# Optimization experiments

Measured on AMD Instinct MI355X. Metric: run time of the kernel, lower is better.

Reference implementation:

```python
import jax, jax.numpy as jnp
import numpy as np

B = 64; PAST = 128; FUTURE = 64; HID = 64; HEADS = 4
F = 16 + 8 + 24 + 3  # out_preprocess = 51


def _pre(cat, num, emb0, emb1, emb2):
    # pre_processing: embedding lookups per categorical column + last 3 float cols
    return jnp.concatenate([emb0[cat[:, 0]], emb1[cat[:, 1]], emb2[cat[:, 2]], num], axis=-1)


def _gat_conv(x, edge_index, lin_w, att_src, att_dst, bias, heads, out_ch):
    # PyG GATConv: concat=False (head mean), add_self_loops=True, leaky_relu slope 0.2
    N = x.shape[0]
    loops = jnp.arange(N, dtype=edge_index.dtype)
    src = jnp.concatenate([edge_index[0], loops])
    dst = jnp.concatenate([edge_index[1], loops])
    h = (x @ lin_w).reshape(N, heads, out_ch)          # [N, H, C]
    a_src = (h * att_src).sum(-1)                      # [N, H]
    a_dst = (h * att_dst).sum(-1)
    e = jax.nn.leaky_relu(a_src[src] + a_dst[dst], 0.2)  # [E, H]
    m = jax.lax.stop_gradient(jax.ops.segment_max(e, dst, num_segments=N))
    ex = jnp.exp(e - m[dst])
    s = jax.ops.segment_sum(ex, dst, num_segments=N)
    alpha = ex / (s[dst] + 1e-16)                      # softmax over in-edges per node
    out = jax.ops.segment_sum(alpha[:, :, None] * h[src], dst, num_segments=N)
    return out.mean(1) + bias                          # concat=False -> mean over heads


def setup_inputs() -> dict:
    ks = jax.random.split(jax.random.key(0), 17)
    N1, N2 = B * PAST, B * FUTURE
    E1, E2 = N1 * 16, N2 * 16
    return dict(
        cat1=jax.random.randint(ks[0], (N1, 3), 0, 7),
        num1=jax.random.normal(ks[1], (N1, 3), dtype=jnp.float32),
        cat2=jax.random.randint(ks[2], (N2, 3), 0, 7),
        num2=jax.random.normal(ks[3], (N2, 3), dtype=jnp.float32),
        e1=jax.random.randint(ks[4], (2, E1), 0, N1),
        e2=jax.random.randint(ks[5], (2, E2), 0, N2),
        A=jax.random.randint(ks[6], (PAST + FUTURE, PAST + FUTURE), 0, 2),
        emb0=0.1 * jax.random.normal(ks[7], (24, 16), dtype=jnp.float32),
        emb1=0.1 * jax.random.normal(ks[8], (7, 8), dtype=jnp.float32),
        emb2=0.1 * jax.random.normal(ks[9], (500, 24), dtype=jnp.float32),
        g1_lin=0.1 * jax.random.normal(ks[10], (F, HEADS * (F - 1)), dtype=jnp.float32),
        g1_asrc=0.1 * jax.random.normal(ks[11], (HEADS, F - 1), dtype=jnp.float32),
        g1_adst=0.1 * jax.random.normal(ks[12], (HEADS, F - 1), dtype=jnp.float32),
        g1_b=jnp.zeros((F - 1,), dtype=jnp.float32),
        g2_lin=0.1 * jax.random.normal(ks[13], (F, HEADS), dtype=jnp.float32),
        g2_asrc=0.1 * jax.random.normal(ks[14], (HEADS, 1), dtype=jnp.float32),
        g2_adst=0.1 * jax.random.normal(ks[15], (HEADS, 1), dtype=jnp.float32),
        g2_b=jnp.zeros((1,), dtype=jnp.float32),
        W=0.1 * jax.random.normal(ks[16], (F - 1, HID), dtype=jnp.float32),
    )


def reference(cat1, num1, cat2, num2, e1, e2, A, emb0, emb1, emb2,
              g1_lin, g1_asrc, g1_adst, g1_b, g2_lin, g2_asrc, g2_adst, g2_b, W):
    x = _pre(cat1, num1, emb0, emb1, emb2)                       # [B*PAST, F]
    x2 = _pre(cat2, num2, emb0, emb1, emb2).reshape(B, FUTURE, F)
    x1 = _gat_conv(x, e1, g1_lin, g1_asrc, g1_adst, g1_b, HEADS, F - 1).reshape(B, PAST, F - 1)
    # pairwise diff between every (future, past) node pair within a graph
    diff = x1[:, None, :, :] - x2[:, :, None, :F - 1]            # [B, FUTURE, PAST, F-1]
    M = W @ W.T
    M = M + M.T                                                  # WW^T + (WW^T)^T
    # original builds full [PAST, PAST] quadratic form and extracts diagonal;
    # compute only the diagonal: -0.5 * diff_i M diff_i
    alpha = -0.5 * jnp.einsum('bfpd,de,bfpe->bfp', diff, M, diff)
    mask = A[:PAST, PAST:].T                                     # [FUTURE, PAST]
    alpha = jnp.where(mask == 0, -jnp.inf, alpha)
    alpha = jax.nn.softmax(alpha, axis=-1)
    y_past = x.reshape(B, PAST, F)[:, :, -1:]                    # [B, PAST, 1]
    tmp = alpha @ y_past                                         # [B, FUTURE, 1]
    x2b = jnp.concatenate([x2[:, :, :F - 1], tmp], axis=-1)
    out = _gat_conv(x2b.reshape(-1, F), e2, g2_lin, g2_asrc, g2_adst, g2_b, HEADS, 1)
    return out.reshape(B, FUTURE)
```

## Files before the change

### kernel.cpp

```cpp
#include <hip/hip_runtime.h>

static constexpr int B_ = 64, PAST = 128, FUTURE = 64, F_ = 51;
static constexpr int N1 = B_ * PAST;
static constexpr int N2 = B_ * FUTURE;
static constexpr int E1 = N1 * 16;
static constexpr int E2 = N2 * 16;
static constexpr int MAXDEG = 64;
static constexpr int CSR_TOT = E1 + N1 + E2 + N2 + FUTURE * PAST;
static constexpr int NB_CSR = CSR_TOT / 256;

__device__ __forceinline__
float node_feat(const int* cat, const float* num, const float* e0, const float* e1,
                const float* e2, int n, int t) {
    if (t < 16) return e0[cat[n * 3 + 0] * 16 + t];
    if (t < 24) return e1[cat[n * 3 + 1] * 8 + (t - 16)];
    if (t < 48) return e2[cat[n * 3 + 2] * 24 + (t - 24)];
    return num[n * 3 + (t - 48)];
}

__global__ __launch_bounds__(256) void k_prep(
        const int* __restrict__ cat1, const float* __restrict__ num1,
        const int* __restrict__ cat2, const float* __restrict__ num2,
        const float* __restrict__ emb0, const float* __restrict__ emb1,
        const float* __restrict__ emb2,
        const float* __restrict__ g1_lin, const float* __restrict__ g1_asrc,
        const float* __restrict__ g1_adst, const float* __restrict__ W,
        const float* __restrict__ g2_lin,
        const int* __restrict__ e1, const int* __restrict__ e2,
        const int* __restrict__ A,
        float* __restrict__ h1, float* __restrict__ asrc1, float* __restrict__ adst1,
        float* __restrict__ y1, float* __restrict__ x2g, float* __restrict__ P2,
        float* __restrict__ h2b,
        int* __restrict__ count1, int* __restrict__ slot1,
        int* __restrict__ count2, int* __restrict__ slot2, int* __restrict__ maskT) {
    int blk = blockIdx.x, t = threadIdx.x;
    if (blk < NB_CSR) {
        int i = blk * 256 + t;
        if (i < E1) {
            int src = e1[i], dst = e1[E1 + i];
            int pos = atomicAdd(&count1[dst], 1);
            if (pos < MAXDEG) slot1[dst * MAXDEG + pos] = src;
        } else if (i < E1 + N1) {
            int n = i - E1;
            int pos = atomicAdd(&count1[n], 1);
            if (pos < MAXDEG) slot1[n * MAXDEG + pos] = n;
        } else if (i < E1 + N1 + E2) {
            int k = i - E1 - N1;
            int src = e2[k], dst = e2[E2 + k];
            int pos = atomicAdd(&count2[dst], 1);
            if (pos < MAXDEG) slot2[dst * MAXDEG + pos] = src;
        } else if (i < E1 + N1 + E2 + N2) {
            int n = i - E1 - N1 - E2;
            int pos = atomicAdd(&count2[n], 1);
            if (pos < MAXDEG) slot2[n * MAXDEG + pos] = n;
        } else if (i < CSR_TOT) {
            int k = i - (E1 + N1 + E2 + N2);
            int f = k >> 7, pp = k & 127;
            maskT[k] = A[pp * 192 + PAST + f];
        }
        return;
    }
    __shared__ float xrow[F_];
    __shared__ float redS[200];
    __shared__ float redD[200];
    int rb = blk - NB_CSR;
    if (rb >= N1) {
        int n = rb - N1;
        if (t < F_) {
            float xv = node_feat(cat2, num2, emb0, emb1, emb2, n, t);
            xrow[t] = xv;
            x2g[n * F_ + t] = xv;
        }
        __syncthreads();
        if (t < 64) {
            float acc = 0.f;
            for (int j = 0; j < 50; ++j) acc += xrow[j] * W[j * 64 + t];
            P2[n * 64 + t] = acc;
        } else if (t < 68) {
            int h = t - 64;
            float acc = 0.f;
            for (int j = 0; j < 50; ++j) acc += xrow[j] * g2_lin[j * 4 + h];
            h2b[n * 4 + h] = acc;
        }
        return;
    }
    int n = rb;
    if (t < F_) {
        float xv = node_feat(cat1, num1, emb0, emb1, emb2, n, t);
        xrow[t] = xv;
        if (t == 50) y1[n] = xv;
    }
    __syncthreads();
    if (t < 200) {
        float acc = 0.f;
        for (int j = 0; j < F_; ++j) acc += xrow[j] * g1_lin[j * 200 + t];
        h1[n * 200 + t] = acc;
        redS[t] = acc * g1_asrc[t];
        redD[t] = acc * g1_adst[t];
    }
    __syncthreads();
    if (t < 4) {
        float s = 0.f;
        for (int c = 0; c < 50; ++c) s += redS[t * 50 + c];
        asrc1[n * 4 + t] = s;
    } else if (t < 8) {
        int h = t - 4;
        float s = 0.f;
        for (int c = 0; c < 50; ++c) s += redD[h * 50 + c];
        adst1[n * 4 + h] = s;
    }
}

__global__ __launch_bounds__(256) void k_gat1(
        const int* __restrict__ count1, const int* __restrict__ slot1,
        const float* __restrict__ h1, const float* __restrict__ asrc1,
        const float* __restrict__ adst1, const float* __restrict__ g1_b,
        const float* __restrict__ W, float* __restrict__ P1T,
        float* __restrict__ n1w) {
    __shared__ int    Ssrc[4][64];
    __shared__ float4 Sw[4][64];
    __shared__ float  Sx[4][64];
    int t = threadIdx.x, lane = t & 63, wv = t >> 6;
    int n = (blockIdx.x * 256 + t) >> 6;
    int deg = min(count1[n], MAXDEG);
    int my_src = (lane < deg) ? slot1[n * MAXDEG + lane] : 0;
    float ad0 = adst1[n * 4 + 0], ad1 = adst1[n * 4 + 1];
    float ad2 = adst1[n * 4 + 2], ad3 = adst1[n * 4 + 3];
    float ex0 = 0.f, ex1 = 0.f, ex2 = 0.f, ex3 = 0.f;
    if (lane < deg) {
        float e0 = asrc1[my_src * 4 + 0] + ad0;
        float e1 = asrc1[my_src * 4 + 1] + ad1;
        float e2 = asrc1[my_src * 4 + 2] + ad2;
        float e3 = asrc1[my_src * 4 + 3] + ad3;
        e0 = e0 >= 0.f ? e0 : 0.2f * e0;  ex0 = __expf(e0);
        e1 = e1 >= 0.f ? e1 : 0.2f * e1;  ex1 = __expf(e1);
        e2 = e2 >= 0.f ? e2 : 0.2f * e2;  ex2 = __expf(e2);
        e3 = e3 >= 0.f ? e3 : 0.2f * e3;  ex3 = __expf(e3);
    }
    float s0 = ex0, s1 = ex1, s2 = ex2, s3 = ex3;
    #pragma unroll
    for (int m = 32; m >= 1; m >>= 1) {
        s0 += __shfl_xor(s0, m);
        s1 += __shfl_xor(s1, m);
        s2 += __shfl_xor(s2, m);
        s3 += __shfl_xor(s3, m);
    }
    Ssrc[wv][lane] = my_src;
    Sw[wv][lane] = make_float4(ex0 / (s0 + 1e-16f), ex1 / (s1 + 1e-16f),
                               ex2 / (s2 + 1e-16f), ex3 / (s3 + 1e-16f));
    __syncthreads();
    float acc0 = 0.f, acc1 = 0.f, acc2 = 0.f, acc3 = 0.f;
    for (int i = 0; i < deg; ++i) {
        int srci = Ssrc[wv][i];
        float4 w = Sw[wv][i];
        if (lane < 50) {
            const float* hr = &h1[srci * 200];
            acc0 += w.x * hr[lane];
            acc1 += w.y * hr[50 + lane];
            acc2 += w.z * hr[100 + lane];
            acc3 += w.w * hr[150 + lane];
        }
    }
    if (lane < 50)
        Sx[wv][lane] = 0.25f * (acc0 + acc1 + acc2 + acc3) + g1_b[lane];
    __syncthreads();
    float a = 0.f;
    for (int j = 0; j < 50; ++j) a += Sx[wv][j] * W[j * 64 + lane];
    int b = n >> 7, p = n & 127;
    P1T[b * 8192 + lane * 128 + p] = a;
    float sq = a * a;
    #pragma unroll
    for (int m = 32; m >= 1; m >>= 1) sq += __shfl_xor(sq, m);
    if (lane == 0) n1w[n] = sq;
}

__global__ __launch_bounds__(256) void k_attn(
        const float* __restrict__ P1T, const float* __restrict__ P2,
        const int* __restrict__ maskT, const float* __restrict__ y1,
        const float* __restrict__ n1w, const float* __restrict__ h2b,
        const float* __restrict__ g2_lin, float* __restrict__ h2g) {
    __shared__ __align__(16) float P1s[8192];
    __shared__ __align__(16) float ys[128];
    __shared__ __align__(16) float n1s[128];
    int b = blockIdx.x >> 4, fg = blockIdx.x & 15;
    int t = threadIdx.x, lane = t & 63, wv = t >> 6;
    const float4* src4 = (const float4*)(P1T + b * 8192);
    float4* dst4 = (float4*)P1s;
    #pragma unroll
    for (int i = 0; i < 8; ++i) dst4[t + i * 256] = src4[t + i * 256];
    if (t < 128) {
        ys[t]  = y1[b * 128 + t];
        n1s[t] = n1w[b * 128 + t];
    }
    __syncthreads();
    int f = (fg << 2) + wv;
    int q = b * 64 + f;
    float p2k = P2[q * 64 + lane];
    float dota = 0.f, dotb = 0.f;
    const float2* P12 = (const float2*)P1s;
    #pragma unroll
    for (int k = 0; k < 64; ++k) {
        float bk = __shfl(p2k, k);
        float2 v = P12[k * 64 + lane];
        dota += v.x * bk;
        dotb += v.y * bk;
    }
    int2  mm  = ((const int2*)maskT)[f * 64 + lane];
    float2 nv = ((const float2*)n1s)[lane];
    float va = mm.x ? (2.f * dota - nv.x) : -1e30f;
    float vb = mm.y ? (2.f * dotb - nv.y) : -1e30f;
    float mx = fmaxf(va, vb);
    #pragma unroll
    for (int m = 32; m >= 1; m >>= 1) mx = fmaxf(mx, __shfl_xor(mx, m));
    float wa = mm.x ? __expf(va - mx) : 0.f;
    float wb = mm.y ? __expf(vb - mx) : 0.f;
    float2 yv = ((const float2*)ys)[lane];
    float sw = wa + wb;
    float sy = wa * yv.x + wb * yv.y;
    #pragma unroll
    for (int m = 32; m >= 1; m >>= 1) {
        sw += __shfl_xor(sw, m);
        sy += __shfl_xor(sy, m);
    }
    float tsh = sy / sw;
    if (lane < 4)
        h2g[q * 4 + lane] = h2b[q * 4 + lane] + tsh * g2_lin[50 * 4 + lane];
}

__global__ __launch_bounds__(256) void k_gat2(
        const int* __restrict__ count2, const int* __restrict__ slot2,
        const float* __restrict__ h2g, const float* __restrict__ g2_asrc,
        const float* __restrict__ g2_adst, const float* __restrict__ g2_b,
        float* __restrict__ out) {
    int wave = (blockIdx.x * blockDim.x + threadIdx.x) >> 6;
    int lane = threadIdx.x & 63;
    if (wave >= N2) return;
    int n = wave;
    int deg = min(count2[n], MAXDEG);
    int my_src = (lane < deg) ? slot2[n * MAXDEG + lane] : 0;
    float ex[4], nm[4], adterm[4], as[4];
    #pragma unroll
    for (int h = 0; h < 4; ++h) {
        as[h] = g2_asrc[h];
        adterm[h] = h2g[n * 4 + h] * g2_adst[h];
        ex[h] = 0.f; nm[h] = 0.f;
    }
    if (lane < deg) {
        #pragma unroll
        for (int h = 0; h < 4; ++h) {
            float hs = h2g[my_src * 4 + h];
            float e = hs * as[h] + adterm[h];
            e = e >= 0.f ? e : 0.2f * e;
            float xv = __expf(e);
            ex[h] = xv;
            nm[h] = xv * hs;
        }
    }
    #pragma unroll
    for (int m = 32; m >= 1; m >>= 1) {
        #pragma unroll
        for (int h = 0; h < 4; ++h) {
            ex[h] += __shfl_xor(ex[h], m);
            nm[h] += __shfl_xor(nm[h], m);
        }
    }
    if (lane == 0) {
        float o = 0.f;
        #pragma unroll
        for (int h = 0; h < 4; ++h) o += nm[h] / (ex[h] + 1e-16f);
        out[n] = 0.25f * o + g2_b[0];
    }
}

extern "C" void kernel_launch(void* const* d_in, const int* in_sizes, int n_in,
                              void* d_out, int out_size, void* d_ws, size_t ws_size,
                              hipStream_t stream) {
    const int*   cat1    = (const int*)  d_in[0];
    const float* num1    = (const float*)d_in[1];
    const int*   cat2    = (const int*)  d_in[2];
    const float* num2    = (const float*)d_in[3];
    const int*   e1      = (const int*)  d_in[4];
    const int*   e2      = (const int*)  d_in[5];
    const int*   A       = (const int*)  d_in[6];
    const float* emb0    = (const float*)d_in[7];
    const float* emb1    = (const float*)d_in[8];
    const float* emb2    = (const float*)d_in[9];
    const float* g1_lin  = (const float*)d_in[10];
    const float* g1_asrc = (const float*)d_in[11];
    const float* g1_adst = (const float*)d_in[12];
    const float* g1_b    = (const float*)d_in[13];
    const float* g2_lin  = (const float*)d_in[14];
    const float* g2_asrc = (const float*)d_in[15];
    const float* g2_adst = (const float*)d_in[16];
    const float* g2_b    = (const float*)d_in[17];
    const float* W       = (const float*)d_in[18];
    float* out = (float*)d_out;

    int*   count1 = (int*)d_ws;
    int*   count2 = count1 + N1;
    int*   slot1  = count2 + N2;
    int*   slot2  = slot1 + N1 * MAXDEG;
    int*   maskT  = slot2 + N2 * MAXDEG;
    float* h1     = (float*)(maskT + FUTURE * PAST);
    float* asrc1  = h1 + N1 * 200;
    float* adst1  = asrc1 + N1 * 4;
    float* y1     = adst1 + N1 * 4;
    float* x2g    = y1 + N1;
    float* P1T    = x2g + N2 * F_;
    float* P2     = P1T + N1 * 64;
    float* h2g    = P2 + N2 * 64;
    float* n1w    = h2g + N2 * 4;
    float* h2b    = n1w + N1;

    hipMemsetAsync(count1, 0, (N1 + N2) * sizeof(int), stream);
    k_prep<<<NB_CSR + N1 + N2, 256, 0, stream>>>(
        cat1, num1, cat2, num2, emb0, emb1, emb2, g1_lin, g1_asrc, g1_adst, W,
        g2_lin, e1, e2, A, h1, asrc1, adst1, y1, x2g, P2, h2b,
        count1, slot1, count2, slot2, maskT);
    k_gat1<<<N1 / 4, 256, 0, stream>>>(count1, slot1, h1, asrc1, adst1, g1_b, W,
                                       P1T, n1w);
    k_attn<<<B_ * 16, 256, 0, stream>>>(P1T, P2, maskT, y1, n1w, h2b, g2_lin, h2g);
    k_gat2<<<N2 / 4, 256, 0, stream>>>(count2, slot2, h2g, g2_asrc, g2_adst, g2_b, out);
}
```

Baseline: 163.6 us.

## Fuse four kernels into one cooperative persistent kernel with grid syncs

Replaces the four separate launches (prep, gat1, attn, gat2) with a single cooperative persistent kernel that walks each phase with grid-stride loops and separates phases with grid.sync(). The goal is to remove per-launch overhead and the inter-kernel gaps. In exchange the grid is capped at 1024 blocks, so each block loops over many nodes, and grid barriers bring their own cost. The unused x2g buffer write is also dropped. If the cooperative launch fails, the code falls back to four persistent launches.

```diff
diff --git a/kernel.cpp b/kernel.cpp
--- a/kernel.cpp
+++ b/kernel.cpp
@@ -1,4 +1,7 @@
 #include <hip/hip_runtime.h>
+#include <hip/hip_cooperative_groups.h>
+
+namespace cg = cooperative_groups;
 
 static constexpr int B_ = 64, PAST = 128, FUTURE = 64, F_ = 51;
 static constexpr int N1 = B_ * PAST;
@@ -6,8 +9,17 @@
 static constexpr int E1 = N1 * 16;
 static constexpr int E2 = N2 * 16;
 static constexpr int MAXDEG = 64;
-static constexpr int CSR_TOT = E1 + N1 + E2 + N2 + FUTURE * PAST;
-static constexpr int NB_CSR = CSR_TOT / 256;
+static constexpr int CSRW = E1 + N1 + E2 + N2;
+static constexpr int MAXGRID = 1024;
+
+struct GArgs {
+    const int *cat1, *cat2, *e1, *e2, *A;
+    const float *num1, *num2, *emb0, *emb1, *emb2;
+    const float *g1_lin, *g1_asrc, *g1_adst, *g1_b;
+    const float *g2_lin, *g2_asrc, *g2_adst, *g2_b, *W;
+    int *count1, *slot1, *count2, *slot2, *maskT;
+    float *h1, *asrc1, *adst1, *y1, *P2, *h2b, *P1T, *n1w, *h2g, *out;
+};
 
 __device__ __forceinline__
 float node_feat(const int* cat, const float* num, const float* e0, const float* e1,
@@ -18,307 +30,326 @@
     return num[n * 3 + (t - 48)];
 }
 
-__global__ __launch_bounds__(256) void k_prep(
-        const int* __restrict__ cat1, const float* __restrict__ num1,
-        const int* __restrict__ cat2, const float* __restrict__ num2,
-        const float* __restrict__ emb0, const float* __restrict__ emb1,
-        const float* __restrict__ emb2,
-        const float* __restrict__ g1_lin, const float* __restrict__ g1_asrc,
-        const float* __restrict__ g1_adst, const float* __restrict__ W,
-        const float* __restrict__ g2_lin,
-        const int* __restrict__ e1, const int* __restrict__ e2,
-        const int* __restrict__ A,
-        float* __restrict__ h1, float* __restrict__ asrc1, float* __restrict__ adst1,
-        float* __restrict__ y1, float* __restrict__ x2g, float* __restrict__ P2,
-        float* __restrict__ h2b,
-        int* __restrict__ count1, int* __restrict__ slot1,
-        int* __restrict__ count2, int* __restrict__ slot2, int* __restrict__ maskT) {
-    int blk = blockIdx.x, t = threadIdx.x;
-    if (blk < NB_CSR) {
-        int i = blk * 256 + t;
+__device__ void phase_prep(const GArgs& a, float* S) {
+    const int t = threadIdx.x, blk = blockIdx.x;
+    const int nthread = gridDim.x * 256;
+    for (int i = blk * 256 + t; i < CSRW + FUTURE * PAST; i += nthread) {
         if (i < E1) {
-            int src = e1[i], dst = e1[E1 + i];
-            int pos = atomicAdd(&count1[dst], 1);
-            if (pos < MAXDEG) slot1[dst * MAXDEG + pos] = src;
+            int src = a.e1[i], dst = a.e1[E1 + i];
+            int pos = atomicAdd(&a.count1[dst], 1);
+            if (pos < MAXDEG) a.slot1[dst * MAXDEG + pos] = src;
         } else if (i < E1 + N1) {
             int n = i - E1;
-            int pos = atomicAdd(&count1[n], 1);
-            if (pos < MAXDEG) slot1[n * MAXDEG + pos] = n;
+            int pos = atomicAdd(&a.count1[n], 1);
+            if (pos < MAXDEG) a.slot1[n * MAXDEG + pos] = n;
         } else if (i < E1 + N1 + E2) {
             int k = i - E1 - N1;
-            int src = e2[k], dst = e2[E2 + k];
-            int pos = atomicAdd(&count2[dst], 1);
-            if (pos < MAXDEG) slot2[dst * MAXDEG + pos] = src;
-        } else if (i < E1 + N1 + E2 + N2) {
+            int src = a.e2[k], dst = a.e2[E2 + k];
+            int pos = atomicAdd(&a.count2[dst], 1);
+            if (pos < MAXDEG) a.slot2[dst * MAXDEG + pos] = src;
+        } else if (i < CSRW) {
             int n = i - E1 - N1 - E2;
-            int pos = atomicAdd(&count2[n], 1);
-            if (pos < MAXDEG) slot2[n * MAXDEG + pos] = n;
-        } else if (i < CSR_TOT) {
-            int k = i - (E1 + N1 + E2 + N2);
+            int pos = atomicAdd(&a.count2[n], 1);
+            if (pos < MAXDEG) a.slot2[n * MAXDEG + pos] = n;
+        } else {
+            int k = i - CSRW;
             int f = k >> 7, pp = k & 127;
-            maskT[k] = A[pp * 192 + PAST + f];
-        }
-        return;
-    }
-    __shared__ float xrow[F_];
-    __shared__ float redS[200];
-    __shared__ float redD[200];
-    int rb = blk - NB_CSR;
-    if (rb >= N1) {
-        int n = rb - N1;
-        if (t < F_) {
-            float xv = node_feat(cat2, num2, emb0, emb1, emb2, n, t);
-            xrow[t] = xv;
-            x2g[n * F_ + t] = xv;
-        }
+            a.maskT[k] = a.A[pp * 192 + PAST + f];
+        }
+    }
+    float* xrow = S;
+    float* redS = S + 64;
+    float* redD = S + 264;
+    for (int vb = blk; vb < N1 + N2; vb += gridDim.x) {
         __syncthreads();
-        if (t < 64) {
-            float acc = 0.f;
-            for (int j = 0; j < 50; ++j) acc += xrow[j] * W[j * 64 + t];
-            P2[n * 64 + t] = acc;
-        } else if (t < 68) {
-            int h = t - 64;
-            float acc = 0.f;
-            for (int j = 0; j < 50; ++j) acc += xrow[j] * g2_lin[j * 4 + h];
-            h2b[n * 4 + h] = acc;
-        }
-        return;
-    }
-    int n = rb;
-    if (t < F_) {
-        float xv = node_feat(cat1, num1, emb0, emb1, emb2, n, t);
-        xrow[t] = xv;
-        if (t == 50) y1[n] = xv;
-    }
-    __syncthreads();
-    if (t < 200) {
-        float acc = 0.f;
-        for (int j = 0; j < F_; ++j) acc += xrow[j] * g1_lin[j * 200 + t];
-        h1[n * 200 + t] = acc;
-        redS[t] = acc * g1_asrc[t];
-        redD[t] = acc * g1_adst[t];
-    }
-    __syncthreads();
-    if (t < 4) {
-        float s = 0.f;
-        for (int c = 0; c < 50; ++c) s += redS[t * 50 + c];
-        asrc1[n * 4 + t] = s;
-    } else if (t < 8) {
-        int h = t - 4;
-        float s = 0.f;
-        for (int c = 0; c < 50; ++c) s += redD[h * 50 + c];
-        adst1[n * 4 + h] = s;
-    }
-}
-
-__global__ __launch_bounds__(256) void k_gat1(
-        const int* __restrict__ count1, const int* __restrict__ slot1,
-        const float* __restrict__ h1, const float* __restrict__ asrc1,
-        const float* __restrict__ adst1, const float* __restrict__ g1_b,
-        const float* __restrict__ W, float* __restrict__ P1T,
-        float* __restrict__ n1w) {
-    __shared__ int    Ssrc[4][64];
-    __shared__ float4 Sw[4][64];
-    __shared__ float  Sx[4][64];
-    int t = threadIdx.x, lane = t & 63, wv = t >> 6;
-    int n = (blockIdx.x * 256 + t) >> 6;
-    int deg = min(count1[n], MAXDEG);
-    int my_src = (lane < deg) ? slot1[n * MAXDEG + lane] : 0;
-    float ad0 = adst1[n * 4 + 0], ad1 = adst1[n * 4 + 1];
-    float ad2 = adst1[n * 4 + 2], ad3 = adst1[n * 4 + 3];
-    float ex0 = 0.f, ex1 = 0.f, ex2 = 0.f, ex3 = 0.f;
-    if (lane < deg) {
-        float e0 = asrc1[my_src * 4 + 0] + ad0;
-        float e1 = asrc1[my_src * 4 + 1] + ad1;
-        float e2 = asrc1[my_src * 4 + 2] + ad2;
-        float e3 = asrc1[my_src * 4 + 3] + ad3;
-        e0 = e0 >= 0.f ? e0 : 0.2f * e0;  ex0 = __expf(e0);
-        e1 = e1 >= 0.f ? e1 : 0.2f * e1;  ex1 = __expf(e1);
-        e2 = e2 >= 0.f ? e2 : 0.2f * e2;  ex2 = __expf(e2);
-        e3 = e3 >= 0.f ? e3 : 0.2f * e3;  ex3 = __expf(e3);
-    }
-    float s0 = ex0, s1 = ex1, s2 = ex2, s3 = ex3;
-    #pragma unroll
-    for (int m = 32; m >= 1; m >>= 1) {
-        s0 += __shfl_xor(s0, m);
-        s1 += __shfl_xor(s1, m);
-        s2 += __shfl_xor(s2, m);
-        s3 += __shfl_xor(s3, m);
-    }
-    Ssrc[wv][lane] = my_src;
-    Sw[wv][lane] = make_float4(ex0 / (s0 + 1e-16f), ex1 / (s1 + 1e-16f),
+        if (vb < N1) {
+            int n = vb;
+            if (t < F_) {
+                float xv = node_feat(a.cat1, a.num1, a.emb0, a.emb1, a.emb2, n, t);
+                xrow[t] = xv;
+                if (t == 50) a.y1[n] = xv;
+            }
+            __syncthreads();
+            if (t < 200) {
+                float acc = 0.f;
+                for (int j = 0; j < F_; ++j) acc += xrow[j] * a.g1_lin[j * 200 + t];
+                a.h1[n * 200 + t] = acc;
+                redS[t] = acc * a.g1_asrc[t];
+                redD[t] = acc * a.g1_adst[t];
+            }
+            __syncthreads();
+            if (t < 4) {
+                float s = 0.f;
+                for (int c = 0; c < 50; ++c) s += redS[t * 50 + c];
+                a.asrc1[n * 4 + t] = s;
+            } else if (t < 8) {
+                int h = t - 4;
+                float s = 0.f;
+                for (int c = 0; c < 50; ++c) s += redD[h * 50 + c];
+                a.adst1[n * 4 + h] = s;
+            }
+        } else {
+            int n = vb - N1;
+            if (t < F_) {
+                float xv = node_feat(a.cat2, a.num2, a.emb0, a.emb1, a.emb2, n, t);
+                xrow[t] = xv;
+            }
+            __syncthreads();
+            if (t < 64) {
+                float acc = 0.f;
+                for (int j = 0; j < 50; ++j) acc += xrow[j] * a.W[j * 64 + t];
+                a.P2[n * 64 + t] = acc;
+            } else if (t < 68) {
+                int h = t - 64;
+                float acc = 0.f;
+                for (int j = 0; j < 50; ++j) acc += xrow[j] * a.g2_lin[j * 4 + h];
+                a.h2b[n * 4 + h] = acc;
+            }
+        }
+    }
+}
+
+__device__ void phase_gat1(const GArgs& a, float* S) {
+    const int t = threadIdx.x, lane = t & 63, wv = t >> 6;
+    int*    Ssrc = (int*)S + wv * 64;
+    float4* Sw   = (float4*)(S + 256) + wv * 64;
+    float*  Sx   = S + 1280 + wv * 64;
+    const int wstride = gridDim.x * 4;
+    for (int n = blockIdx.x * 4 + wv; n < N1; n += wstride) {
+        int deg = min(a.count1[n], MAXDEG);
+        int my_src = (lane < deg) ? a.slot1[n * MAXDEG + lane] : 0;
+        float ad0 = a.adst1[n * 4 + 0], ad1 = a.adst1[n * 4 + 1];
+        float ad2 = a.adst1[n * 4 + 2], ad3 = a.adst1[n * 4 + 3];
+        float ex0 = 0.f, ex1 = 0.f, ex2 = 0.f, ex3 = 0.f;
+        if (lane < deg) {
+            float e0 = a.asrc1[my_src * 4 + 0] + ad0;
+            float e1 = a.asrc1[my_src * 4 + 1] + ad1;
+            float e2 = a.asrc1[my_src * 4 + 2] + ad2;
+            float e3 = a.asrc1[my_src * 4 + 3] + ad3;
+            e0 = e0 >= 0.f ? e0 : 0.2f * e0;  ex0 = __expf(e0);
+            e1 = e1 >= 0.f ? e1 : 0.2f * e1;  ex1 = __expf(e1);
+            e2 = e2 >= 0.f ? e2 : 0.2f * e2;  ex2 = __expf(e2);
+            e3 = e3 >= 0.f ? e3 : 0.2f * e3;  ex3 = __expf(e3);
+        }
+        float s0 = ex0, s1 = ex1, s2 = ex2, s3 = ex3;
+        #pragma unroll
+        for (int m = 32; m >= 1; m >>= 1) {
+            s0 += __shfl_xor(s0, m);
+            s1 += __shfl_xor(s1, m);
+            s2 += __shfl_xor(s2, m);
+            s3 += __shfl_xor(s3, m);
+        }
+        Ssrc[lane] = my_src;
+        Sw[lane] = make_float4(ex0 / (s0 + 1e-16f), ex1 / (s1 + 1e-16f),
                                ex2 / (s2 + 1e-16f), ex3 / (s3 + 1e-16f));
-    __syncthreads();
-    float acc0 = 0.f, acc1 = 0.f, acc2 = 0.f, acc3 = 0.f;
-    for (int i = 0; i < deg; ++i) {
-        int srci = Ssrc[wv][i];
-        float4 w = Sw[wv][i];
-        if (lane < 50) {
-            const float* hr = &h1[srci * 200];
-            acc0 += w.x * hr[lane];
-            acc1 += w.y * hr[50 + lane];
-            acc2 += w.z * hr[100 + lane];
-            acc3 += w.w * hr[150 + lane];
-        }
-    }
-    if (lane < 50)
-        Sx[wv][lane] = 0.25f * (acc0 + acc1 + acc2 + acc3) + g1_b[lane];
-    __syncthreads();
-    float a = 0.f;
-    for (int j = 0; j < 50; ++j) a += Sx[wv][j] * W[j * 64 + lane];
-    int b = n >> 7, p = n & 127;
-    P1T[b * 8192 + lane * 128 + p] = a;
-    float sq = a * a;
-    #pragma unroll
-    for (int m = 32; m >= 1; m >>= 1) sq += __shfl_xor(sq, m);
-    if (lane == 0) n1w[n] = sq;
-}
-
-__global__ __launch_bounds__(256) void k_attn(
-        const float* __restrict__ P1T, const float* __restrict__ P2,
-        const int* __restrict__ maskT, const float* __restrict__ y1,
-        const float* __restrict__ n1w, const float* __restrict__ h2b,
-        const float* __restrict__ g2_lin, float* __restrict__ h2g) {
-    __shared__ __align__(16) float P1s[8192];
-    __shared__ __align__(16) float ys[128];
-    __shared__ __align__(16) float n1s[128];
-    int b = blockIdx.x >> 4, fg = blockIdx.x & 15;
-    int t = threadIdx.x, lane = t & 63, wv = t >> 6;
-    const float4* src4 = (const float4*)(P1T + b * 8192);
-    float4* dst4 = (float4*)P1s;
-    #pragma unroll
-    for (int i = 0; i < 8; ++i) dst4[t + i * 256] = src4[t + i * 256];
-    if (t < 128) {
-        ys[t]  = y1[b * 128 + t];
-        n1s[t] = n1w[b * 128 + t];
-    }
-    __syncthreads();
-    int f = (fg << 2) + wv;
-    int q = b * 64 + f;
-    float p2k = P2[q * 64 + lane];
-    float dota = 0.f, dotb = 0.f;
-    const float2* P12 = (const float2*)P1s;
-    #pragma unroll
-    for (int k = 0; k < 64; ++k) {
-        float bk = __shfl(p2k, k);
-        float2 v = P12[k * 64 + lane];
-        dota += v.x * bk;
-        dotb += v.y * bk;
-    }
-    int2  mm  = ((const int2*)maskT)[f * 64 + lane];
-    float2 nv = ((const float2*)n1s)[lane];
-    float va = mm.x ? (2.f * dota - nv.x) : -1e30f;
-    float vb = mm.y ? (2.f * dotb - nv.y) : -1e30f;
-    float mx = fmaxf(va, vb);
-    #pragma unroll
-    for (int m = 32; m >= 1; m >>= 1) mx = fmaxf(mx, __shfl_xor(mx, m));
-    float wa = mm.x ? __expf(va - mx) : 0.f;
-    float wb = mm.y ? __expf(vb - mx) : 0.f;
-    float2 yv = ((const float2*)ys)[lane];
-    float sw = wa + wb;
-    float sy = wa * yv.x + wb * yv.y;
-    #pragma unroll
-    for (int m = 32; m >= 1; m >>= 1) {
-        sw += __shfl_xor(sw, m);
-        sy += __shfl_xor(sy, m);
-    }
-    float tsh = sy / sw;
-    if (lane < 4)
-        h2g[q * 4 + lane] = h2b[q * 4 + lane] + tsh * g2_lin[50 * 4 + lane];
-}
-
-__global__ __launch_bounds__(256) void k_gat2(
-        const int* __restrict__ count2, const int* __restrict__ slot2,
-        const float* __restrict__ h2g, const float* __restrict__ g2_asrc,
-        const float* __restrict__ g2_adst, const float* __restrict__ g2_b,
-        float* __restrict__ out) {
-    int wave = (blockIdx.x * blockDim.x + threadIdx.x) >> 6;
-    int lane = threadIdx.x & 63;
-    if (wave >= N2) return;
-    int n = wave;
-    int deg = min(count2[n], MAXDEG);
-    int my_src = (lane < deg) ? slot2[n * MAXDEG + lane] : 0;
-    float ex[4], nm[4], adterm[4], as[4];
-    #pragma unroll
-    for (int h = 0; h < 4; ++h) {
-        as[h] = g2_asrc[h];
-        adterm[h] = h2g[n * 4 + h] * g2_adst[h];
-        ex[h] = 0.f; nm[h] = 0.f;
-    }
-    if (lane < deg) {
+        float acc0 = 0.f, acc1 = 0.f, acc2 = 0.f, acc3 = 0.f;
+        for (int i = 0; i < deg; ++i) {
+            int srci = Ssrc[i];
+            float4 w = Sw[i];
+            if (lane < 50) {
+                const float* hr = &a.h1[srci * 200];
+                acc0 += w.x * hr[lane];
+                acc1 += w.y * hr[50 + lane];
+                acc2 += w.z * hr[100 + lane];
+                acc3 += w.w * hr[150 + lane];
+            }
+        }
+        if (lane < 50)
+            Sx[lane] = 0.25f * (acc0 + acc1 + acc2 + acc3) + a.g1_b[lane];
+        float av = 0.f;
+        for (int j = 0; j < 50; ++j) av += Sx[j] * a.W[j * 64 + lane];
+        int b = n >> 7, p = n & 127;
+        a.P1T[b * 8192 + lane * 128 + p] = av;
+        float sq = av * av;
+        #pragma unroll
+        for (int m = 32; m >= 1; m >>= 1) sq += __shfl_xor(sq, m);
+        if (lane == 0) a.n1w[n] = sq;
+    }
+}
+
+__device__ void phase_attn(const GArgs& a, float* S) {
+    float* P1s = S;
+    float* ys  = S + 8192;
+    float* n1s = S + 8320;
+    const int t = threadIdx.x, lane = t & 63, wv = t >> 6;
+    for (int task = blockIdx.x; task < B_ * 16; task += gridDim.x) {
+        __syncthreads();
+        int b = task >> 4, fg = task & 15;
+        const float4* src4 = (const float4*)(a.P1T + b * 8192);
+        float4* dst4 = (float4*)P1s;
+        #pragma unroll
+        for (int i = 0; i < 8; ++i) dst4[t + i * 256] = src4[t + i * 256];
+        if (t < 128) {
+            ys[t]  = a.y1[b * 128 + t];
+            n1s[t] = a.n1w[b * 128 + t];
+        }
+        __syncthreads();
+        int f = (fg << 2) + wv;
+        int q = b * 64 + f;
+        float p2k = a.P2[q * 64 + lane];
+        float dota = 0.f, dotb = 0.f;
+        const float2* P12 = (const float2*)P1s;
+        #pragma unroll
+        for (int k = 0; k < 64; ++k) {
+            float bk = __shfl(p2k, k);
+            float2 v = P12[k * 64 + lane];
+            dota += v.x * bk;
+            dotb += v.y * bk;
+        }
+        int2  mm = ((const int2*)a.maskT)[f * 64 + lane];
+        float2 nv = ((const float2*)n1s)[lane];
+        float sva = mm.x ? (2.f * dota - nv.x) : -1e30f;
+        float svb = mm.y ? (2.f * dotb - nv.y) : -1e30f;
+        float mx = fmaxf(sva, svb);
+        #pragma unroll
+        for (int m = 32; m >= 1; m >>= 1) mx = fmaxf(mx, __shfl_xor(mx, m));
+        float wa = mm.x ? __expf(sva - mx) : 0.f;
+        float wb = mm.y ? __expf(svb - mx) : 0.f;
+        float2 yv = ((const float2*)ys)[lane];
+        float sw = wa + wb;
+        float sy = wa * yv.x + wb * yv.y;
+        #pragma unroll
+        for (int m = 32; m >= 1; m >>= 1) {
+            sw += __shfl_xor(sw, m);
+            sy += __shfl_xor(sy, m);
+        }
+        float tsh = sy / sw;
+        if (lane < 4)
+            a.h2g[q * 4 + lane] = a.h2b[q * 4 + lane] + tsh * a.g2_lin[200 + lane];
+    }
+}
+
+__device__ void phase_gat2(const GArgs& a) {
+    const int t = threadIdx.x, lane = t & 63, wv = t >> 6;
+    for (int n = blockIdx.x * 4 + wv; n < N2; n += gridDim.x * 4) {
+        int deg = min(a.count2[n], MAXDEG);
+        int my_src = (lane < deg) ? a.slot2[n * MAXDEG + lane] : 0;
+        float ex[4], nm[4], adterm[4], as[4];
         #pragma unroll
         for (int h = 0; h < 4; ++h) {
-            float hs = h2g[my_src * 4 + h];
-            float e = hs * as[h] + adterm[h];
-            e = e >= 0.f ? e : 0.2f * e;
-            float xv = __expf(e);
-            ex[h] = xv;
-            nm[h] = xv * hs;
-        }
-    }
-    #pragma unroll
-    for (int m = 32; m >= 1; m >>= 1) {
-        #pragma unroll
-        for (int h = 0; h < 4; ++h) {
-            ex[h] += __shfl_xor(ex[h], m);
-            nm[h] += __shfl_xor(nm[h], m);
-        }
-    }
-    if (lane == 0) {
-        float o = 0.f;
-        #pragma unroll
-        for (int h = 0; h < 4; ++h) o += nm[h] / (ex[h] + 1e-16f);
-        out[n] = 0.25f * o + g2_b[0];
-    }
+            as[h] = a.g2_asrc[h];
+            adterm[h] = a.h2g[n * 4 + h] * a.g2_adst[h];
+            ex[h] = 0.f; nm[h] = 0.f;
+        }
+        if (lane < deg) {
+            #pragma unroll
+            for (int h = 0; h < 4; ++h) {
+                float hs = a.h2g[my_src * 4 + h];
+                float e = hs * as[h] + adterm[h];
+                e = e >= 0.f ? e : 0.2f * e;
+                float xv = __expf(e);
+                ex[h] = xv;
+                nm[h] = xv * hs;
+            }
+        }
+        #pragma unroll
+        for (int m = 32; m >= 1; m >>= 1) {
+            #pragma unroll
+            for (int h = 0; h < 4; ++h) {
+                ex[h] += __shfl_xor(ex[h], m);
+                nm[h] += __shfl_xor(nm[h], m);
+            }
+        }
+        if (lane == 0) {
+            float o = 0.f;
+            #pragma unroll
+            for (int h = 0; h < 4; ++h) o += nm[h] / (ex[h] + 1e-16f);
+            a.out[n] = 0.25f * o + a.g2_b[0];
+        }
+    }
+}
+
+__global__ __launch_bounds__(256, 4) void k_mega(GArgs a) {
+    cg::grid_group grid = cg::this_grid();
+    __shared__ __align__(16) float S[8448];
+    phase_prep(a, S);
+    grid.sync();
+    phase_gat1(a, S);
+    grid.sync();
+    phase_attn(a, S);
+    grid.sync();
+    phase_gat2(a);
+}
+
+__global__ __launch_bounds__(256, 4) void k_p1(GArgs a) {
+    __shared__ __align__(16) float S[8448];
+    phase_prep(a, S);
+}
+__global__ __launch_bounds__(256, 4) void k_p2(GArgs a) {
+    __shared__ __align__(16) float S[8448];
+    phase_gat1(a, S);
+}
+__global__ __launch_bounds__(256, 4) void k_p3(GArgs a) {
+    __shared__ __align__(16) float S[8448];
+    phase_attn(a, S);
+}
+__global__ __launch_bounds__(256, 4) void k_p4(GArgs a) {
+    phase_gat2(a);
 }
 
 extern "C" void kernel_launch(void* const* d_in, const int* in_sizes, int n_in,
                               void* d_out, int out_size, void* d_ws, size_t ws_size,
                               hipStream_t stream) {
-    const int*   cat1    = (const int*)  d_in[0];
-    const float* num1    = (const float*)d_in[1];
-    const int*   cat2    = (const int*)  d_in[2];
-    const float* num2    = (const float*)d_in[3];
-    const int*   e1      = (const int*)  d_in[4];
-    const int*   e2      = (const int*)  d_in[5];
-    const int*   A       = (const int*)  d_in[6];
-    const float* emb0    = (const float*)d_in[7];
-    const float* emb1    = (const float*)d_in[8];
-    const float* emb2    = (const float*)d_in[9];
-    const float* g1_lin  = (const float*)d_in[10];
-    const float* g1_asrc = (const float*)d_in[11];
-    const float* g1_adst = (const float*)d_in[12];
-    const float* g1_b    = (const float*)d_in[13];
-    const float* g2_lin  = (const float*)d_in[14];
-    const float* g2_asrc = (const float*)d_in[15];
-    const float* g2_adst = (const float*)d_in[16];
-    const float* g2_b    = (const float*)d_in[17];
-    const float* W       = (const float*)d_in[18];
-    float* out = (float*)d_out;
-
-    int*   count1 = (int*)d_ws;
-    int*   count2 = count1 + N1;
-    int*   slot1  = count2 + N2;
-    int*   slot2  = slot1 + N1 * MAXDEG;
-    int*   maskT  = slot2 + N2 * MAXDEG;
-    float* h1     = (float*)(maskT + FUTURE * PAST);
-    float* asrc1  = h1 + N1 * 200;
-    float* adst1  = asrc1 + N1 * 4;
-    float* y1     = adst1 + N1 * 4;
-    float* x2g    = y1 + N1;
-    float* P1T    = x2g + N2 * F_;
-    float* P2     = P1T + N1 * 64;
-    float* h2g    = P2 + N2 * 64;
-    float* n1w    = h2g + N2 * 4;
-    float* h2b    = n1w + N1;
-
-    hipMemsetAsync(count1, 0, (N1 + N2) * sizeof(int), stream);
-    k_prep<<<NB_CSR + N1 + N2, 256, 0, stream>>>(
-        cat1, num1, cat2, num2, emb0, emb1, emb2, g1_lin, g1_asrc, g1_adst, W,
-        g2_lin, e1, e2, A, h1, asrc1, adst1, y1, x2g, P2, h2b,
-        count1, slot1, count2, slot2, maskT);
-    k_gat1<<<N1 / 4, 256, 0, stream>>>(count1, slot1, h1, asrc1, adst1, g1_b, W,
-                                       P1T, n1w);
-    k_attn<<<B_ * 16, 256, 0, stream>>>(P1T, P2, maskT, y1, n1w, h2b, g2_lin, h2g);
-    k_gat2<<<N2 / 4, 256, 0, stream>>>(count2, slot2, h2g, g2_asrc, g2_adst, g2_b, out);
-}
+    GArgs a;
+    a.cat1    = (const int*)  d_in[0];
+    a.num1    = (const float*)d_in[1];
+    a.cat2    = (const int*)  d_in[2];
+    a.num2    = (const float*)d_in[3];
+    a.e1      = (const int*)  d_in[4];
+    a.e2      = (const int*)  d_in[5];
+    a.A       = (const int*)  d_in[6];
+    a.emb0    = (const float*)d_in[7];
+    a.emb1    = (const float*)d_in[8];
+    a.emb2    = (const float*)d_in[9];
+    a.g1_lin  = (const float*)d_in[10];
+    a.g1_asrc = (const float*)d_in[11];
+    a.g1_adst = (const float*)d_in[12];
+    a.g1_b    = (const float*)d_in[13];
+    a.g2_lin  = (const float*)d_in[14];
+    a.g2_asrc = (const float*)d_in[15];
+    a.g2_adst = (const float*)d_in[16];
+    a.g2_b    = (const float*)d_in[17];
+    a.W       = (const float*)d_in[18];
+
+    a.count1 = (int*)d_ws;
+    a.count2 = a.count1 + N1;
+    a.slot1  = a.count2 + N2;
+    a.slot2  = a.slot1 + N1 * MAXDEG;
+    a.maskT  = a.slot2 + N2 * MAXDEG;
+    a.h1     = (float*)(a.maskT + FUTURE * PAST);
+    a.asrc1  = a.h1 + N1 * 200;
+    a.adst1  = a.asrc1 + N1 * 4;
+    a.y1     = a.adst1 + N1 * 4;
+    a.P1T    = a.y1 + N1;
+    a.P2     = a.P1T + N1 * 64;
+    a.h2b    = a.P2 + N2 * 64;
+    a.h2g    = a.h2b + N2 * 4;
+    a.n1w    = a.h2g + N2 * 4;
+    a.out    = (float*)d_out;
+
+    static int grid_blocks = 0;
+    if (grid_blocks == 0) {
+        int per_cu = 0;
+        if (hipOccupancyMaxActiveBlocksPerMultiprocessor(&per_cu, k_mega, 256, 0)
+                != hipSuccess || per_cu < 1)
+            per_cu = 4;
+        int dev = 0, ncu = 0;
+        hipGetDevice(&dev);
+        if (hipDeviceGetAttribute(&ncu, hipDeviceAttributeMultiprocessorCount, dev)
+                != hipSuccess || ncu < 1)
+            ncu = 256;
+        long g = (long)per_cu * (long)ncu;
+        grid_blocks = (int)(g > MAXGRID ? MAXGRID : g);
+    }
+
+    hipMemsetAsync(a.count1, 0, (N1 + N2) * sizeof(int), stream);
+    void* kargs[] = { (void*)&a };
+    hipError_t err = hipLaunchCooperativeKernel(k_mega, dim3(grid_blocks), dim3(256),
+                                                kargs, 0, stream);
+    if (err != hipSuccess) {
+        k_p1<<<MAXGRID, 256, 0, stream>>>(a);
+        k_p2<<<MAXGRID, 256, 0, stream>>>(a);
+        k_p3<<<MAXGRID, 256, 0, stream>>>(a);
+        k_p4<<<MAXGRID, 256, 0, stream>>>(a);
+    }
+}
```

Measured after the change: 497.3 us. +204.0%, slower.
